# Optimization experiments

Measured on AMD Instinct MI355X. Metric: run time of the kernel, lower is better.

## Reference

```python
import jax, jax.numpy as jnp
import numpy as np

WIN = 7                 # skimage default win_size (gaussian_weights=False)
K1, K2 = 0.01, 0.03     # skimage defaults
DATA_RANGE = 2.0        # skimage dtype range for float images: dmax - dmin = 1 - (-1)


def _uniform_filter_valid(x):
    """7x7 uniform (mean) filter, VALID padding, depthwise over channels.
    x: [B, C, H, W] -> [B, C, H-6, W-6]. Equivalent to skimage uniform_filter
    followed by crop(pad) since reflected borders are discarded."""
    C = x.shape[1]
    k = jnp.full((C, 1, WIN, WIN), 1.0 / (WIN * WIN), dtype=x.dtype)
    return jax.lax.conv_general_dilated(
        x, k, window_strides=(1, 1), padding='VALID',
        dimension_numbers=('NCHW', 'OIHW', 'NCHW'),
        feature_group_count=C)


def _ssim_mean(pred, target):
    N = WIN * WIN
    cov_norm = N / (N - 1.0)  # sample covariance (skimage use_sample_covariance=True)
    ux = _uniform_filter_valid(pred)
    uy = _uniform_filter_valid(target)
    uxx = _uniform_filter_valid(pred * pred)
    uyy = _uniform_filter_valid(target * target)
    uxy = _uniform_filter_valid(pred * target)
    vx = cov_norm * (uxx - ux * ux)
    vy = cov_norm * (uyy - uy * uy)
    vxy = cov_norm * (uxy - ux * uy)
    C1 = (K1 * DATA_RANGE) ** 2
    C2 = (K2 * DATA_RANGE) ** 2
    S = ((2.0 * ux * uy + C1) * (2.0 * vxy + C2)) / (
        (ux * ux + uy * uy + C1) * (vx + vy + C2))
    # equal-weight mean over channels / images == global mean of valid map
    return jnp.mean(S)


def setup_inputs() -> dict:
    key = jax.random.key(0)
    k1, k2 = jax.random.split(key)
    shape = (32, 3, 512, 512)
    pred = jax.random.uniform(k1, shape, dtype=jnp.float32)
    target = jax.random.uniform(k2, shape, dtype=jnp.float32)
    return {"pred": pred, "target": target}


def reference(pred, target):
    return 1.0 - _ssim_mean(pred, target)
```

## Files before the change

kernel.cpp:

```cpp
#include <hip/hip_runtime.h>

#define IMG     512
#define VALID   506
#define NPLANES 96
#define R       16
#define BANDS   32

__device__ __forceinline__ float shfl_next(float v, int baddr) {
    return __int_as_float(__builtin_amdgcn_ds_bpermute(baddr, __float_as_int(v)));
}

__device__ __forceinline__ void addv(float4& V, const float4 p) {
    V.x += p.x; V.y += p.y; V.z += p.z; V.w += p.w;
}
__device__ __forceinline__ void subv(float4& V, const float4 p) {
    V.x -= p.x; V.y -= p.y; V.z -= p.z; V.w -= p.w;
}
__device__ __forceinline__ void addmul(float4& V, const float4 p, const float4 q) {
    V.x = fmaf(p.x, q.x, V.x); V.y = fmaf(p.y, q.y, V.y);
    V.z = fmaf(p.z, q.z, V.z); V.w = fmaf(p.w, q.w, V.w);
}
__device__ __forceinline__ void submul(float4& V, const float4 p, const float4 q) {
    V.x = fmaf(-p.x, q.x, V.x); V.y = fmaf(-p.y, q.y, V.y);
    V.z = fmaf(-p.z, q.z, V.z); V.w = fmaf(-p.w, q.w, V.w);
}

__device__ __forceinline__ void hsum7(const float4 A, const float4 B, int baddr, float o[8]) {
    float n0 = shfl_next(A.x, baddr);
    float n1 = shfl_next(A.y, baddr);
    float n2 = shfl_next(A.z, baddr);
    float n3 = shfl_next(A.w, baddr);
    float n4 = shfl_next(B.x, baddr);
    float n5 = shfl_next(B.y, baddr);
    o[0] = ((A.x + A.y) + (A.z + A.w)) + ((B.x + B.y) + B.z);
    o[1] = (o[0] - A.x) + B.w;
    o[2] = (o[1] - A.y) + n0;
    o[3] = (o[2] - A.z) + n1;
    o[4] = (o[3] - A.w) + n2;
    o[5] = (o[4] - B.x) + n3;
    o[6] = (o[5] - B.y) + n4;
    o[7] = (o[6] - B.z) + n5;
}

#define LOADROW(x0, x1, y0, y1, r) do {                                         \
    const float4* _p = reinterpret_cast<const float4*>(pp + (size_t)(r) * IMG); \
    const float4* _q = reinterpret_cast<const float4*>(pt + (size_t)(r) * IMG); \
    x0 = _p[0]; x1 = _p[1]; y0 = _q[0]; y1 = _q[1]; } while (0)

__global__ __launch_bounds__(256, 3) void ssim_wave_kernel(
    const float* __restrict__ pred,
    const float* __restrict__ target,
    double* __restrict__ accum)
{
    __shared__ float wsum[4];

    const int t     = threadIdx.x;
    const int lane  = t & 63;
    const int wv    = t >> 6;
    const int band  = blockIdx.x * 4 + wv;
    const int plane = blockIdx.y;
    const int row0  = band * R;
    const int col   = lane << 3;

    const size_t pbase = (size_t)plane * (IMG * IMG);
    const float* __restrict__ pp = pred   + pbase + col;
    const float* __restrict__ pt = target + pbase + col;

    const int baddr = ((lane + 1) & 63) << 2;

    float4 z = make_float4(0.f, 0.f, 0.f, 0.f);
    float4 Vx_a = z, Vx_b = z, Vy_a = z, Vy_b = z;
    float4 Vxx_a = z, Vxx_b = z, Vyy_a = z, Vyy_b = z, Vxy_a = z, Vxy_b = z;

    float4 nx0, nx1, ny0, ny1;
    LOADROW(nx0, nx1, ny0, ny1, row0);

    #pragma unroll 2
    for (int k = 0; k < 6; ++k) {
        float4 px0 = nx0, px1 = nx1, py0 = ny0, py1 = ny1;
        LOADROW(nx0, nx1, ny0, ny1, row0 + k + 1);
        addv(Vx_a, px0);  addv(Vx_b, px1);
        addv(Vy_a, py0);  addv(Vy_b, py1);
        addmul(Vxx_a, px0, px0); addmul(Vxx_b, px1, px1);
        addmul(Vyy_a, py0, py0); addmul(Vyy_b, py1, py1);
        addmul(Vxy_a, px0, py0); addmul(Vxy_b, px1, py1);
    }

    const float c1 = 0.9604f;
    const float c2 = 8.4672f;
    float local = 0.f;

    #pragma unroll 2
    for (int i = 0; i < R; ++i) {
        float4 px0 = nx0, px1 = nx1, py0 = ny0, py1 = ny1;

        float4 ox0, ox1, oy0, oy1;
        const bool has_old = (i > 0);
        if (has_old) LOADROW(ox0, ox1, oy0, oy1, row0 + i - 1);

        int rn = row0 + 7 + i; rn = rn < IMG - 1 ? rn : IMG - 1;
        LOADROW(nx0, nx1, ny0, ny1, rn);

        addv(Vx_a, px0);  addv(Vx_b, px1);
        addv(Vy_a, py0);  addv(Vy_b, py1);
        addmul(Vxx_a, px0, px0); addmul(Vxx_b, px1, px1);
        addmul(Vyy_a, py0, py0); addmul(Vyy_b, py1, py1);
        addmul(Vxy_a, px0, py0); addmul(Vxy_b, px1, py1);
        if (has_old) {
            subv(Vx_a, ox0);  subv(Vx_b, ox1);
            subv(Vy_a, oy0);  subv(Vy_b, oy1);
            submul(Vxx_a, ox0, ox0); submul(Vxx_b, ox1, ox1);
            submul(Vyy_a, oy0, oy0); submul(Vyy_b, oy1, oy1);
            submul(Vxy_a, ox0, oy0); submul(Vxy_b, ox1, oy1);
        }

        const bool row_ok = (row0 + i) < VALID;
        if (row_ok) {
            float hx[8], hy[8], hxx[8], hyy[8], hxy[8];
            hsum7(Vx_a,  Vx_b,  baddr, hx);
            hsum7(Vy_a,  Vy_b,  baddr, hy);
            hsum7(Vxx_a, Vxx_b, baddr, hxx);
            hsum7(Vyy_a, Vyy_b, baddr, hyy);
            hsum7(Vxy_a, Vxy_b, baddr, hxy);
            #pragma unroll
            for (int j = 0; j < 8; ++j) {
                float t1 = hx[j] * hy[j];
                float t2 = fmaf(hx[j], hx[j], hy[j] * hy[j]);
                float n1 = fmaf(2.f, t1, c1);
                float d1 = t2 + c1;
                float n2 = fmaf(-2.f, t1, fmaf(98.f, hxy[j], c2));
                float d2 = fmaf(49.f, hxx[j] + hyy[j], c2) - t2;
                float S  = __fdividef(n1 * n2, d1 * d2);
                local += (col + j < VALID) ? S : 0.f;
            }
        }
    }

    #pragma unroll
    for (int off = 32; off > 0; off >>= 1)
        local += __shfl_down(local, off, 64);
    if (lane == 0) wsum[wv] = local;
    __syncthreads();
    if (t == 0)
        atomicAdd(accum, (double)(wsum[0] + wsum[1] + wsum[2] + wsum[3]));
}

__global__ void ssim_finalize_kernel(const double* __restrict__ accum,
                                     float* __restrict__ out)
{
    const double n_valid = (double)NPLANES * (double)VALID * (double)VALID;
    out[0] = (float)(1.0 - accum[0] / n_valid);
}

extern "C" void kernel_launch(void* const* d_in, const int* in_sizes, int n_in,
                              void* d_out, int out_size, void* d_ws, size_t ws_size,
                              hipStream_t stream) {
    const float* pred   = (const float*)d_in[0];
    const float* target = (const float*)d_in[1];
    float* out = (float*)d_out;
    double* accum = (double*)d_ws;

    hipMemsetAsync(d_ws, 0, sizeof(double), stream);

    dim3 grid(BANDS / 4, NPLANES);
    ssim_wave_kernel<<<grid, 256, 0, stream>>>(pred, target, accum);
    ssim_finalize_kernel<<<1, 1, 0, stream>>>(accum, out);
}
```

Baseline: 82.53 us.

## Merge xx/yy sums, halve band height, prefetch old rows, fully unroll

The per-pixel x² and y² running sums are combined into one accumulator, because the SSIM denominator only uses their sum. This removes one horizontal shuffle-sum and several FMAs per row. Band height drops from 16 to 8 rows and the grid doubles, which raises parallelism but adds more warm-up rows per output row. Old rows are now loaded one iteration ahead into registers, the loops are fully unrolled, and the occupancy hint in launch_bounds is removed. These changes may raise register pressure.

```diff
diff --git a/kernel.cpp b/kernel.cpp
--- a/kernel.cpp
+++ b/kernel.cpp
@@ -3,8 +3,8 @@
 #define IMG     512
 #define VALID   506
 #define NPLANES 96
-#define R       16
-#define BANDS   32
+#define R       8
+#define NBANDS  64
 
 __device__ __forceinline__ float shfl_next(float v, int baddr) {
     return __int_as_float(__builtin_amdgcn_ds_bpermute(baddr, __float_as_int(v)));
@@ -47,7 +47,7 @@
     const float4* _q = reinterpret_cast<const float4*>(pt + (size_t)(r) * IMG); \
     x0 = _p[0]; x1 = _p[1]; y0 = _q[0]; y1 = _q[1]; } while (0)
 
-__global__ __launch_bounds__(256, 3) void ssim_wave_kernel(
+__global__ __launch_bounds__(256) void ssim_wave_kernel(
     const float* __restrict__ pred,
     const float* __restrict__ target,
     double* __restrict__ accum)
@@ -70,57 +70,59 @@
 
     float4 z = make_float4(0.f, 0.f, 0.f, 0.f);
     float4 Vx_a = z, Vx_b = z, Vy_a = z, Vy_b = z;
-    float4 Vxx_a = z, Vxx_b = z, Vyy_a = z, Vyy_b = z, Vxy_a = z, Vxy_b = z;
+    float4 Vss_a = z, Vss_b = z, Vxy_a = z, Vxy_b = z;
 
     float4 nx0, nx1, ny0, ny1;
     LOADROW(nx0, nx1, ny0, ny1, row0);
 
-    #pragma unroll 2
+    #pragma unroll
     for (int k = 0; k < 6; ++k) {
         float4 px0 = nx0, px1 = nx1, py0 = ny0, py1 = ny1;
         LOADROW(nx0, nx1, ny0, ny1, row0 + k + 1);
         addv(Vx_a, px0);  addv(Vx_b, px1);
         addv(Vy_a, py0);  addv(Vy_b, py1);
-        addmul(Vxx_a, px0, px0); addmul(Vxx_b, px1, px1);
-        addmul(Vyy_a, py0, py0); addmul(Vyy_b, py1, py1);
+        addmul(Vss_a, px0, px0); addmul(Vss_b, px1, px1);
+        addmul(Vss_a, py0, py0); addmul(Vss_b, py1, py1);
         addmul(Vxy_a, px0, py0); addmul(Vxy_b, px1, py1);
     }
+
+    float4 pox0, pox1, poy0, poy1;
+    LOADROW(pox0, pox1, poy0, poy1, row0);
 
     const float c1 = 0.9604f;
     const float c2 = 8.4672f;
     float local = 0.f;
 
-    #pragma unroll 2
+    #pragma unroll
     for (int i = 0; i < R; ++i) {
         float4 px0 = nx0, px1 = nx1, py0 = ny0, py1 = ny1;
+        float4 ox0 = pox0, ox1 = pox1, oy0 = poy0, oy1 = poy1;
 
-        float4 ox0, ox1, oy0, oy1;
-        const bool has_old = (i > 0);
-        if (has_old) LOADROW(ox0, ox1, oy0, oy1, row0 + i - 1);
-
-        int rn = row0 + 7 + i; rn = rn < IMG - 1 ? rn : IMG - 1;
-        LOADROW(nx0, nx1, ny0, ny1, rn);
+        if (i < R - 1) {
+            int rn = row0 + 7 + i; rn = rn < IMG - 1 ? rn : IMG - 1;
+            LOADROW(nx0, nx1, ny0, ny1, rn);
+            if (i > 0) LOADROW(pox0, pox1, poy0, poy1, row0 + i);
+        }
 
         addv(Vx_a, px0);  addv(Vx_b, px1);
         addv(Vy_a, py0);  addv(Vy_b, py1);
-        addmul(Vxx_a, px0, px0); addmul(Vxx_b, px1, px1);
-        addmul(Vyy_a, py0, py0); addmul(Vyy_b, py1, py1);
+        addmul(Vss_a, px0, px0); addmul(Vss_b, px1, px1);
+        addmul(Vss_a, py0, py0); addmul(Vss_b, py1, py1);
         addmul(Vxy_a, px0, py0); addmul(Vxy_b, px1, py1);
-        if (has_old) {
+        if (i > 0) {
             subv(Vx_a, ox0);  subv(Vx_b, ox1);
             subv(Vy_a, oy0);  subv(Vy_b, oy1);
-            submul(Vxx_a, ox0, ox0); submul(Vxx_b, ox1, ox1);
-            submul(Vyy_a, oy0, oy0); submul(Vyy_b, oy1, oy1);
+            submul(Vss_a, ox0, ox0); submul(Vss_b, ox1, ox1);
+            submul(Vss_a, oy0, oy0); submul(Vss_b, oy1, oy1);
             submul(Vxy_a, ox0, oy0); submul(Vxy_b, ox1, oy1);
         }
 
         const bool row_ok = (row0 + i) < VALID;
         if (row_ok) {
-            float hx[8], hy[8], hxx[8], hyy[8], hxy[8];
+            float hx[8], hy[8], hss[8], hxy[8];
             hsum7(Vx_a,  Vx_b,  baddr, hx);
             hsum7(Vy_a,  Vy_b,  baddr, hy);
-            hsum7(Vxx_a, Vxx_b, baddr, hxx);
-            hsum7(Vyy_a, Vyy_b, baddr, hyy);
+            hsum7(Vss_a, Vss_b, baddr, hss);
             hsum7(Vxy_a, Vxy_b, baddr, hxy);
             #pragma unroll
             for (int j = 0; j < 8; ++j) {
@@ -129,7 +131,7 @@
                 float n1 = fmaf(2.f, t1, c1);
                 float d1 = t2 + c1;
                 float n2 = fmaf(-2.f, t1, fmaf(98.f, hxy[j], c2));
-                float d2 = fmaf(49.f, hxx[j] + hyy[j], c2) - t2;
+                float d2 = fmaf(49.f, hss[j], c2) - t2;
                 float S  = __fdividef(n1 * n2, d1 * d2);
                 local += (col + j < VALID) ? S : 0.f;
             }
@@ -162,7 +164,7 @@
 
     hipMemsetAsync(d_ws, 0, sizeof(double), stream);
 
-    dim3 grid(BANDS / 4, NPLANES);
+    dim3 grid(NBANDS / 4, NPLANES);
     ssim_wave_kernel<<<grid, 256, 0, stream>>>(pred, target, accum);
     ssim_finalize_kernel<<<1, 1, 0, stream>>>(accum, out);
 }
```

Result: faster. 72.48 us (-12.2%).
